# Optimization experiments

Measured on AMD Instinct MI355X. Metric: run time of the kernel, lower is better.

Reference implementation:

```python
import jax, jax.numpy as jnp
import numpy as np
from jax import lax

N = 4194304  # batch of FP16 values, each encoded as 16 spike bits

# MSB-first bit weights / shift amounts for the [S,E4..E0,M9..M0] layout
_POW = np.array([1 << (15 - i) for i in range(16)], dtype=np.int32)
_SHIFTS = np.array([15 - i for i in range(16)], dtype=np.int32)


def _pack(bits):
    """[..., 16] {0,1} float bits (MSB first) -> float16 scalar per row."""
    b = jnp.round(bits).astype(jnp.int32)
    u = jnp.sum(b * _POW, axis=-1).astype(jnp.uint16)
    return lax.bitcast_convert_type(u, jnp.float16)


def _unpack(f):
    """float16 [...] -> [..., 16] {0,1} float32 bits (MSB first)."""
    u = lax.bitcast_convert_type(f, jnp.uint16).astype(jnp.int32)
    return ((u[..., None] >> _SHIFTS) & 1).astype(jnp.float32)


def _sample_bits(key, n):
    bits = jax.random.bernoulli(key, 0.5, (n, 16)).astype(jnp.float32)
    # avoid exponent == 31 (Inf/NaN encodings) so outputs are well-defined finite fp16
    all_ones = jnp.prod(bits[:, 1:6], axis=-1, keepdims=True)
    return bits.at[:, 5:6].set(bits[:, 5:6] * (1.0 - all_ones))


def setup_inputs() -> dict:
    key = jax.random.key(0)
    ka, kb = jax.random.split(key)
    return {"A": _sample_bits(ka, N), "B": _sample_bits(kb, N)}


def reference(A, B):
    # The SNN gate network implements an IEEE-754 FP16 adder (round-to-nearest-even,
    # subnormal support, overflow/underflow handling) over bit-encoded operands.
    # fp16 add computed via fp32 is bit-exact here (24 >= 2*11+2, Figueroa's theorem),
    # which is what XLA does for float16 on CPU.
    s = _pack(A) + _pack(B)
    return _unpack(s)
```

## Files before the change

kernel.cpp:

```cpp
#include <hip/hip_runtime.h>
#include <hip/hip_fp16.h>


typedef float fx4 __attribute__((ext_vector_type(4)));

__global__ __launch_bounds__(256) void spike_fp16_add_kernel(
    const uint4* __restrict__ A, const uint4* __restrict__ B,
    float4* __restrict__ O, int nf4)
{
    const int lane = threadIdx.x & 63;
    const int waveBase = ((blockIdx.x * blockDim.x + threadIdx.x) >> 6) * 256;
    const int q  = lane & 3;
    const int sh = 12 - 4 * q;

    if (waveBase + 256 <= nf4) {
        uint4 a[4], b[4];
        #pragma unroll
        for (int k = 0; k < 4; ++k) {
            a[k] = A[waveBase + k * 64 + lane];
            b[k] = B[waveBase + k * 64 + lane];
        }

        #pragma unroll
        for (int k = 0; k < 4; ++k) {
            uint32_t na = ((a[k].x >> 20) & 8u) | ((a[k].y >> 21) & 4u) |
                          ((a[k].z >> 22) & 2u) | ((a[k].w >> 23) & 1u);
            uint32_t nb = ((b[k].x >> 20) & 8u) | ((b[k].y >> 21) & 4u) |
                          ((b[k].z >> 22) & 2u) | ((b[k].w >> 23) & 1u);

            uint32_t w = (na << sh) | (nb << (sh + 16));

            w |= (uint32_t)__builtin_amdgcn_mov_dpp((int)w, 0xB1, 0xF, 0xF, true);
            w |= (uint32_t)__builtin_amdgcn_mov_dpp((int)w, 0x4E, 0xF, 0xF, true);

            float fa = __half2float(__ushort_as_half((unsigned short)(w & 0xFFFFu)));
            float fb = __half2float(__ushort_as_half((unsigned short)(w >> 16)));
            uint32_t us = (uint32_t)__half_as_ushort(__float2half_rn(fa + fb));

            uint32_t ns = (us >> sh) & 0xFu;
            fx4 o;
            o.x = (float)((ns >> 3) & 1u);
            o.y = (float)((ns >> 2) & 1u);
            o.z = (float)((ns >> 1) & 1u);
            o.w = (float)( ns       & 1u);

            __builtin_nontemporal_store(
                o, (fx4*)&O[waveBase + k * 64 + lane]);
        }
    } else {
        #pragma unroll
        for (int k = 0; k < 4; ++k) {
            const int f4 = waveBase + k * 64 + lane;
            if (f4 >= nf4) continue;

            uint4 a = A[f4];
            uint4 b = B[f4];
            uint32_t na = ((a.x >> 20) & 8u) | ((a.y >> 21) & 4u) |
                          ((a.z >> 22) & 2u) | ((a.w >> 23) & 1u);
            uint32_t nb = ((b.x >> 20) & 8u) | ((b.y >> 21) & 4u) |
                          ((b.z >> 22) & 2u) | ((b.w >> 23) & 1u);
            uint32_t w = (na << sh) | (nb << (sh + 16));
            w |= (uint32_t)__shfl_xor((int)w, 1);
            w |= (uint32_t)__shfl_xor((int)w, 2);

            float fa = __half2float(__ushort_as_half((unsigned short)(w & 0xFFFFu)));
            float fb = __half2float(__ushort_as_half((unsigned short)(w >> 16)));
            uint32_t us = (uint32_t)__half_as_ushort(__float2half_rn(fa + fb));

            uint32_t ns = (us >> sh) & 0xFu;
            float4 o;
            o.x = (float)((ns >> 3) & 1u);
            o.y = (float)((ns >> 2) & 1u);
            o.z = (float)((ns >> 1) & 1u);
            o.w = (float)( ns       & 1u);
            O[f4] = o;
        }
    }
}

extern "C" void kernel_launch(void* const* d_in, const int* in_sizes, int n_in,
                              void* d_out, int out_size, void* d_ws, size_t ws_size,
                              hipStream_t stream) {
    const uint4* A = (const uint4*)d_in[0];
    const uint4* B = (const uint4*)d_in[1];
    float4* O = (float4*)d_out;

    int nf4 = in_sizes[0] / 4;
    int block = 256;
    int threads = (nf4 + 3) / 4;
    int grid = (threads + block - 1) / block;
    spike_fp16_add_kernel<<<grid, block, 0, stream>>>(A, B, O, nf4);
}
```

Baseline: 584.9 us.

## Use fixed-size grid with per-wave contiguous chunk loop and plain stores

Replaces the one-chunk-per-wave launch with a fixed grid of 2048 blocks where each wave processes a contiguous range of 256-float4 chunks in a loop, with the last wave handling any tail. Nontemporal stores are replaced by ordinary stores. This is meant to reduce block launch/scheduling overhead. In exchange, each wave has fewer independent loads in flight across iterations, and the output may now pollute cache.

New measurement: 583.2 us. About the same (-0.3%).

```diff
diff --git a/kernel.cpp b/kernel.cpp
--- a/kernel.cpp
+++ b/kernel.cpp
@@ -1,32 +1,39 @@
 #include <hip/hip_runtime.h>
 #include <hip/hip_fp16.h>
 
-
-typedef float fx4 __attribute__((ext_vector_type(4)));
 
 __global__ __launch_bounds__(256) void spike_fp16_add_kernel(
     const uint4* __restrict__ A, const uint4* __restrict__ B,
     float4* __restrict__ O, int nf4)
 {
-    const int lane = threadIdx.x & 63;
-    const int waveBase = ((blockIdx.x * blockDim.x + threadIdx.x) >> 6) * 256;
-    const int q  = lane & 3;
-    const int sh = 12 - 4 * q;
+    const int lane   = threadIdx.x & 63;
+    const int wid    = (blockIdx.x * blockDim.x + threadIdx.x) >> 6;
+    const int nWaves = (gridDim.x * blockDim.x) >> 6;
+    const int q      = lane & 3;
+    const int sh     = 12 - 4 * q;
 
-    if (waveBase + 256 <= nf4) {
-        uint4 a[4], b[4];
-        #pragma unroll
-        for (int k = 0; k < 4; ++k) {
-            a[k] = A[waveBase + k * 64 + lane];
-            b[k] = B[waveBase + k * 64 + lane];
-        }
+    const int nChunks = nf4 >> 8;
+    const int cpw     = (nChunks + nWaves - 1) / nWaves;
+    const int c0      = wid * cpw;
+    const int c1      = (c0 + cpw < nChunks) ? c0 + cpw : nChunks;
+
+    for (int c = c0; c < c1; ++c) {
+        const int base = (c << 8) + lane;
+
+        uint4 a0 = A[base      ], a1 = A[base +  64],
+              a2 = A[base + 128], a3 = A[base + 192];
+        uint4 b0 = B[base      ], b1 = B[base +  64],
+              b2 = B[base + 128], b3 = B[base + 192];
+
+        uint4 av[4] = {a0, a1, a2, a3};
+        uint4 bv[4] = {b0, b1, b2, b3};
 
         #pragma unroll
         for (int k = 0; k < 4; ++k) {
-            uint32_t na = ((a[k].x >> 20) & 8u) | ((a[k].y >> 21) & 4u) |
-                          ((a[k].z >> 22) & 2u) | ((a[k].w >> 23) & 1u);
-            uint32_t nb = ((b[k].x >> 20) & 8u) | ((b[k].y >> 21) & 4u) |
-                          ((b[k].z >> 22) & 2u) | ((b[k].w >> 23) & 1u);
+            uint32_t na = ((av[k].x >> 20) & 8u) | ((av[k].y >> 21) & 4u) |
+                          ((av[k].z >> 22) & 2u) | ((av[k].w >> 23) & 1u);
+            uint32_t nb = ((bv[k].x >> 20) & 8u) | ((bv[k].y >> 21) & 4u) |
+                          ((bv[k].z >> 22) & 2u) | ((bv[k].w >> 23) & 1u);
 
             uint32_t w = (na << sh) | (nb << (sh + 16));
 
@@ -38,21 +45,20 @@
             uint32_t us = (uint32_t)__half_as_ushort(__float2half_rn(fa + fb));
 
             uint32_t ns = (us >> sh) & 0xFu;
-            fx4 o;
+            float4 o;
             o.x = (float)((ns >> 3) & 1u);
             o.y = (float)((ns >> 2) & 1u);
             o.z = (float)((ns >> 1) & 1u);
             o.w = (float)( ns       & 1u);
 
-            __builtin_nontemporal_store(
-                o, (fx4*)&O[waveBase + k * 64 + lane]);
+            O[base + k * 64] = o;
         }
-    } else {
-        #pragma unroll
-        for (int k = 0; k < 4; ++k) {
-            const int f4 = waveBase + k * 64 + lane;
-            if (f4 >= nf4) continue;
+    }
 
+    const int tailStart = nChunks << 8;
+    if (tailStart < nf4 && wid == nWaves - 1) {
+        for (int f4 = tailStart + lane; ; f4 += 64) {
+            if (f4 >= nf4) break;
             uint4 a = A[f4];
             uint4 b = B[f4];
             uint32_t na = ((a.x >> 20) & 8u) | ((a.y >> 21) & 4u) |
@@ -86,8 +92,11 @@
     float4* O = (float4*)d_out;
 
     int nf4 = in_sizes[0] / 4;
+
     int block = 256;
-    int threads = (nf4 + 3) / 4;
-    int grid = (threads + block - 1) / block;
+    int nChunks = nf4 >> 8;
+    int grid = 2048;
+    if (grid > nChunks && nChunks > 0) grid = nChunks;
+    if (grid < 1) grid = 1;
     spike_fp16_add_kernel<<<grid, block, 0, stream>>>(A, B, O, nf4);
 }
```
